# Optimization experiments

Hardware: AMD Instinct MI355X
Metric: run time of the kernel (lower is better)

Reference implementation:

```python
import jax, jax.numpy as jnp
import numpy as np

EPS = 1e-5
TOP_K = 2


def setup_inputs() -> dict:
    key = jax.random.key(0)
    ks = jax.random.split(key, 6)
    T, H, F, E = 4096, 1024, 2816, 8
    scale = 0.02
    return {
        "hidden_states": jax.random.normal(ks[0], (T, H), dtype=jnp.float32),
        "ln_w": jnp.ones((H,), dtype=jnp.float32),
        "router_w": jax.random.normal(ks[1], (H, E), dtype=jnp.float32) * scale,
        "w_gate": jax.random.normal(ks[2], (E, H, F), dtype=jnp.float32) * scale,
        "w_up": jax.random.normal(ks[3], (E, H, F), dtype=jnp.float32) * scale,
        "w_down": jax.random.normal(ks[4], (E, F, H), dtype=jnp.float32) * scale,
    }


def reference(hidden_states, ln_w, router_w, w_gate, w_up, w_down):
    # RMSNorm (LlamaRMSNorm)
    var = jnp.mean(hidden_states * hidden_states, axis=-1, keepdims=True)
    x = hidden_states * jax.lax.rsqrt(var + EPS) * ln_w  # [T, H]

    # TopKRouter: softmax over experts, then top-k probs/indices
    logits = x @ router_w                     # [T, E]
    probs = jax.nn.softmax(logits, axis=-1)
    topk_p, topk_i = jax.lax.top_k(probs, TOP_K)  # [T, K]

    # Dense combine weights [T, E]: prob for routed experts, 0 otherwise
    T = x.shape[0]
    combine = jnp.zeros_like(probs).at[jnp.arange(T)[:, None], topk_i].add(topk_p)

    # Experts: Llama-style gated MLP (SwiGLU); loop over fixed small expert set
    out = jnp.zeros_like(x)
    for e in range(w_gate.shape[0]):
        h = jax.nn.silu(x @ w_gate[e]) * (x @ w_up[e])   # [T, F]
        out = out + combine[:, e:e + 1] * (h @ w_down[e])
    return out
```

## Files before the change

### kernel.cpp

```cpp
#include <hip/hip_runtime.h>

#define T_TOK 4096
#define H_DIM 1024
#define F_DIM 2816
#define E_NUM 8
#define EPSV 1e-5f

typedef unsigned short u16;
typedef __attribute__((ext_vector_type(8))) short bf16x8;
typedef __attribute__((ext_vector_type(4))) float f32x4;

__device__ __forceinline__ u16 f2bf(float f) {
  union { float f; unsigned u; } c; c.f = f;
  unsigned u = c.u;
  return (u16)((u + 0x7FFFu + ((u >> 16) & 1u)) >> 16);
}

__global__ __launch_bounds__(256) void router_kernel(
    const float* __restrict__ hs, const float* __restrict__ lnw,
    const float* __restrict__ rw, u16* __restrict__ x_h,
    int* __restrict__ cnt, int* __restrict__ list,
    float* __restrict__ wcomb, int* __restrict__ slot) {
  const int wave = threadIdx.x >> 6;
  const int lane = threadIdx.x & 63;
  const int t = blockIdx.x * 4 + wave;
  const float* row = hs + (size_t)t * H_DIM;

  float4 v[4];
  float ss = 0.f;
#pragma unroll
  for (int j = 0; j < 4; ++j) {
    v[j] = ((const float4*)row)[j * 64 + lane];
    ss += v[j].x * v[j].x + v[j].y * v[j].y + v[j].z * v[j].z + v[j].w * v[j].w;
  }
#pragma unroll
  for (int m = 32; m; m >>= 1) ss += __shfl_xor(ss, m, 64);
  const float inv = rsqrtf(ss * (1.0f / H_DIM) + EPSV);

  float lg[E_NUM];
#pragma unroll
  for (int e = 0; e < E_NUM; ++e) lg[e] = 0.f;

#pragma unroll
  for (int j = 0; j < 4; ++j) {
    const int idx = j * 64 + lane;
    const int h0 = idx * 4;
    float4 w4 = ((const float4*)lnw)[idx];
    float xv[4] = {v[j].x * inv * w4.x, v[j].y * inv * w4.y,
                   v[j].z * inv * w4.z, v[j].w * inv * w4.w};
    ushort4 xs;
    xs.x = f2bf(xv[0]); xs.y = f2bf(xv[1]); xs.z = f2bf(xv[2]); xs.w = f2bf(xv[3]);
    ((ushort4*)(x_h + (size_t)t * H_DIM))[idx] = xs;
#pragma unroll
    for (int q = 0; q < 4; ++q) {
      const float* rr = rw + (size_t)(h0 + q) * E_NUM;
      float4 a = ((const float4*)rr)[0];
      float4 b = ((const float4*)rr)[1];
      lg[0] += xv[q] * a.x; lg[1] += xv[q] * a.y;
      lg[2] += xv[q] * a.z; lg[3] += xv[q] * a.w;
      lg[4] += xv[q] * b.x; lg[5] += xv[q] * b.y;
      lg[6] += xv[q] * b.z; lg[7] += xv[q] * b.w;
    }
  }
#pragma unroll
  for (int e = 0; e < E_NUM; ++e)
#pragma unroll
    for (int m = 32; m; m >>= 1) lg[e] += __shfl_xor(lg[e], m, 64);

  if (lane == 0) {
    float mx = lg[0];
#pragma unroll
    for (int e = 1; e < E_NUM; ++e) mx = fmaxf(mx, lg[e]);
    float p[E_NUM], s = 0.f;
#pragma unroll
    for (int e = 0; e < E_NUM; ++e) { p[e] = __expf(lg[e] - mx); s += p[e]; }
    const float invs = 1.0f / s;
    int e1 = 0; float b1 = p[0];
#pragma unroll
    for (int e = 1; e < E_NUM; ++e) if (p[e] > b1) { b1 = p[e]; e1 = e; }
    int e2 = -1; float b2 = -1.f;
#pragma unroll
    for (int e = 0; e < E_NUM; ++e) if (e != e1 && p[e] > b2) { b2 = p[e]; e2 = e; }
    b1 *= invs; b2 *= invs;
    int p1 = atomicAdd(&cnt[e1], 1);
    list[e1 * T_TOK + p1] = t; wcomb[e1 * T_TOK + p1] = b1;
    slot[2 * t] = (e1 << 16) | p1;
    int p2 = atomicAdd(&cnt[e2], 1);
    list[e2 * T_TOK + p2] = t; wcomb[e2 * T_TOK + p2] = b2;
    slot[2 * t + 1] = (e2 << 16) | p2;
  }
}

__global__ void offsets_kernel(const int* __restrict__ cnt, int* __restrict__ offs) {
  if (threadIdx.x == 0) {
    int s = 0;
    for (int e = 0; e < E_NUM; ++e) { offs[e] = s; s += cnt[e]; }
  }
}

__global__ __launch_bounds__(256) void transpose_cvt(
    const float* __restrict__ in, u16* __restrict__ out, int R, int C) {
  __shared__ float tile[32][33];
  const size_t base = (size_t)blockIdx.z * R * C;
  const int c0 = blockIdx.x * 32, r0 = blockIdx.y * 32;
  const int tx = threadIdx.x, ty = threadIdx.y;
#pragma unroll
  for (int j = 0; j < 32; j += 8)
    tile[ty + j][tx] = in[base + (size_t)(r0 + ty + j) * C + c0 + tx];
  __syncthreads();
#pragma unroll
  for (int j = 0; j < 32; j += 8)
    out[base + (size_t)(c0 + ty + j) * R + r0 + tx] = f2bf(tile[tx][ty + j]);
}

__global__ __launch_bounds__(256) void gemm1_kernel(
    const u16* __restrict__ x_h, const u16* __restrict__ wgT,
    const u16* __restrict__ wuT, const int* __restrict__ cnt,
    const int* __restrict__ offs, const int* __restrict__ list,
    u16* __restrict__ hbuf) {
  const int e = blockIdx.z;
  const int n_e = cnt[e];
  const int rt = blockIdx.y;
  if (rt * 128 >= n_e) return;
  const int ft = blockIdx.x;

  __shared__ __align__(16) u16 As[128][72];
  __shared__ __align__(16) u16 Bgs[64][72];
  __shared__ __align__(16) u16 Bus[64][72];
  __shared__ int tok[128];

  const int tid = threadIdx.x;
  if (tid < 128) {
    int r = rt * 128 + tid;
    if (r >= n_e) r = n_e - 1;
    tok[tid] = list[e * T_TOK + r];
  }
  __syncthreads();

  const int wv = tid >> 6, lane = tid & 63;
  const int wm = wv >> 1, wn = wv & 1;
  const int lrow = lane & 15, quad = lane >> 4;

  f32x4 accg[4][2], accu[4][2];
#pragma unroll
  for (int i = 0; i < 4; ++i)
#pragma unroll
    for (int j = 0; j < 2; ++j) {
      accg[i][j] = f32x4{0.f, 0.f, 0.f, 0.f};
      accu[i][j] = f32x4{0.f, 0.f, 0.f, 0.f};
    }

  const size_t wb = ((size_t)e * F_DIM + (size_t)ft * 64) * H_DIM;

  for (int k0 = 0; k0 < H_DIM; k0 += 64) {
#pragma unroll
    for (int i = 0; i < 4; ++i) {
      int c = tid + i * 256;
      int r = c >> 3, kc = (c & 7) << 3;
      *(uint4*)&As[r][kc] = *(const uint4*)(x_h + (size_t)tok[r] * H_DIM + k0 + kc);
    }
#pragma unroll
    for (int i = 0; i < 2; ++i) {
      int c = tid + i * 256;
      int fr = c >> 3, kc = (c & 7) << 3;
      size_t g = wb + (size_t)fr * H_DIM + k0 + kc;
      *(uint4*)&Bgs[fr][kc] = *(const uint4*)(wgT + g);
      *(uint4*)&Bus[fr][kc] = *(const uint4*)(wuT + g);
    }
    __syncthreads();
#pragma unroll
    for (int ks = 0; ks < 2; ++ks) {
      const int kk = ks * 32 + quad * 8;
      bf16x8 a[4], bg[2], bu[2];
#pragma unroll
      for (int tm = 0; tm < 4; ++tm)
        a[tm] = *(const bf16x8*)&As[wm * 64 + tm * 16 + lrow][kk];
#pragma unroll
      for (int tn = 0; tn < 2; ++tn) {
        bg[tn] = *(const bf16x8*)&Bgs[wn * 32 + tn * 16 + lrow][kk];
        bu[tn] = *(const bf16x8*)&Bus[wn * 32 + tn * 16 + lrow][kk];
      }
#pragma unroll
      for (int tm = 0; tm < 4; ++tm)
#pragma unroll
        for (int tn = 0; tn < 2; ++tn) {
          accg[tm][tn] = __builtin_amdgcn_mfma_f32_16x16x32_bf16(a[tm], bg[tn], accg[tm][tn], 0, 0, 0);
          accu[tm][tn] = __builtin_amdgcn_mfma_f32_16x16x32_bf16(a[tm], bu[tn], accu[tm][tn], 0, 0, 0);
        }
    }
    __syncthreads();
  }

  const int oe = offs[e];
#pragma unroll
  for (int tm = 0; tm < 4; ++tm) {
    const int lr0 = wm * 64 + tm * 16 + quad * 4;
#pragma unroll
    for (int rr = 0; rr < 4; ++rr) {
      const int gr = rt * 128 + lr0 + rr;
      if (gr < n_e) {
#pragma unroll
        for (int tn = 0; tn < 2; ++tn) {
          float g = accg[tm][tn][rr];
          float u = accu[tm][tn][rr];
          float hv = g / (1.0f + __expf(-g)) * u;
          int col = ft * 64 + wn * 32 + tn * 16 + lrow;
          hbuf[(size_t)(oe + gr) * F_DIM + col] = f2bf(hv);
        }
      }
    }
  }
}

__global__ __launch_bounds__(256) void gemm2_kernel(
    const u16* __restrict__ hbuf, const u16* __restrict__ wdT,
    const int* __restrict__ cnt, const int* __restrict__ offs,
    const float* __restrict__ wcomb, float* __restrict__ contrib) {
  const int e = blockIdx.z;
  const int n_e = cnt[e];
  const int rt = blockIdx.y;
  if (rt * 128 >= n_e) return;
  const int nt = blockIdx.x;

  __shared__ __align__(16) u16 As[128][72];
  __shared__ __align__(16) u16 Bs[64][72];
  __shared__ int hrow[128];

  const int tid = threadIdx.x;
  const int oe = offs[e];
  if (tid < 128) {
    int r = rt * 128 + tid;
    if (r >= n_e) r = n_e - 1;
    hrow[tid] = oe + r;
  }
  __syncthreads();

  const int wv = tid >> 6, lane = tid & 63;
  const int wm = wv >> 1, wn = wv & 1;
  const int lrow = lane & 15, quad = lane >> 4;

  f32x4 acc[4][2];
#pragma unroll
  for (int i = 0; i < 4; ++i)
#pragma unroll
    for (int j = 0; j < 2; ++j) acc[i][j] = f32x4{0.f, 0.f, 0.f, 0.f};

  const size_t wb = ((size_t)e * H_DIM + (size_t)nt * 64) * F_DIM;

  for (int k0 = 0; k0 < F_DIM; k0 += 64) {
#pragma unroll
    for (int i = 0; i < 4; ++i) {
      int c = tid + i * 256;
      int r = c >> 3, kc = (c & 7) << 3;
      *(uint4*)&As[r][kc] = *(const uint4*)(hbuf + (size_t)hrow[r] * F_DIM + k0 + kc);
    }
#pragma unroll
    for (int i = 0; i < 2; ++i) {
      int c = tid + i * 256;
      int fr = c >> 3, kc = (c & 7) << 3;
      *(uint4*)&Bs[fr][kc] = *(const uint4*)(wdT + wb + (size_t)fr * F_DIM + k0 + kc);
    }
    __syncthreads();
#pragma unroll
    for (int ks = 0; ks < 2; ++ks) {
      const int kk = ks * 32 + quad * 8;
      bf16x8 a[4], b[2];
#pragma unroll
      for (int tm = 0; tm < 4; ++tm)
        a[tm] = *(const bf16x8*)&As[wm * 64 + tm * 16 + lrow][kk];
#pragma unroll
      for (int tn = 0; tn < 2; ++tn)
        b[tn] = *(const bf16x8*)&Bs[wn * 32 + tn * 16 + lrow][kk];
#pragma unroll
      for (int tm = 0; tm < 4; ++tm)
#pragma unroll
        for (int tn = 0; tn < 2; ++tn)
          acc[tm][tn] = __builtin_amdgcn_mfma_f32_16x16x32_bf16(a[tm], b[tn], acc[tm][tn], 0, 0, 0);
    }
    __syncthreads();
  }

#pragma unroll
  for (int tm = 0; tm < 4; ++tm) {
    const int lr0 = wm * 64 + tm * 16 + quad * 4;
#pragma unroll
    for (int rr = 0; rr < 4; ++rr) {
      const int gr = rt * 128 + lr0 + rr;
      if (gr < n_e) {
        const float cw = wcomb[e * T_TOK + gr];
#pragma unroll
        for (int tn = 0; tn < 2; ++tn) {
          int col = nt * 64 + wn * 32 + tn * 16 + lrow;
          contrib[(size_t)(oe + gr) * H_DIM + col] = acc[tm][tn][rr] * cw;
        }
      }
    }
  }
}

__global__ __launch_bounds__(256) void combine_kernel(
    const float* __restrict__ contrib, const int* __restrict__ offs,
    const int* __restrict__ slot, float* __restrict__ out) {
  const int t = blockIdx.x;
  const int s0 = slot[2 * t], s1 = slot[2 * t + 1];
  const int r0 = offs[s0 >> 16] + (s0 & 0xFFFF);
  const int r1 = offs[s1 >> 16] + (s1 & 0xFFFF);
  float4 a = ((const float4*)(contrib + (size_t)r0 * H_DIM))[threadIdx.x];
  float4 b = ((const float4*)(contrib + (size_t)r1 * H_DIM))[threadIdx.x];
  float4 o = {a.x + b.x, a.y + b.y, a.z + b.z, a.w + b.w};
  ((float4*)(out + (size_t)t * H_DIM))[threadIdx.x] = o;
}

extern "C" void kernel_launch(void* const* d_in, const int* in_sizes, int n_in,
                              void* d_out, int out_size, void* d_ws, size_t ws_size,
                              hipStream_t stream) {
  const float* hs  = (const float*)d_in[0];
  const float* lnw = (const float*)d_in[1];
  const float* rw  = (const float*)d_in[2];
  const float* wg  = (const float*)d_in[3];
  const float* wu  = (const float*)d_in[4];
  const float* wd  = (const float*)d_in[5];
  float* out = (float*)d_out;

  char* p = (char*)d_ws;
  const size_t SZ_XH = (size_t)T_TOK * H_DIM * 2;
  const size_t SZ_W  = (size_t)E_NUM * F_DIM * H_DIM * 2;
  const size_t SZ_HB = (size_t)T_TOK * 2 * F_DIM * 2;
  const size_t SZ_CT = (size_t)T_TOK * 2 * H_DIM * 4;

  u16* x_h  = (u16*)p;   p += SZ_XH;
  u16* wgT  = (u16*)p;   p += SZ_W;
  u16* wuT  = (u16*)p;   p += SZ_W;
  u16* wdT  = (u16*)p;   p += SZ_W;
  u16* hbuf = (u16*)p;   p += SZ_HB;
  float* contrib = (float*)p; p += SZ_CT;
  int* cnt  = (int*)p;   p += 256;
  int* offs = (int*)p;   p += 256;
  int* list = (int*)p;   p += (size_t)E_NUM * T_TOK * 4;
  float* wcomb = (float*)p; p += (size_t)E_NUM * T_TOK * 4;
  int* slot = (int*)p;   p += (size_t)T_TOK * 2 * 4;

  hipMemsetAsync(cnt, 0, 256, stream);
  router_kernel<<<T_TOK / 4, 256, 0, stream>>>(hs, lnw, rw, x_h, cnt, list, wcomb, slot);
  offsets_kernel<<<1, 64, 0, stream>>>(cnt, offs);
  transpose_cvt<<<dim3(F_DIM / 32, H_DIM / 32, E_NUM), dim3(32, 8), 0, stream>>>(wg, wgT, H_DIM, F_DIM);
  transpose_cvt<<<dim3(F_DIM / 32, H_DIM / 32, E_NUM), dim3(32, 8), 0, stream>>>(wu, wuT, H_DIM, F_DIM);
  transpose_cvt<<<dim3(H_DIM / 32, F_DIM / 32, E_NUM), dim3(32, 8), 0, stream>>>(wd, wdT, F_DIM, H_DIM);
  gemm1_kernel<<<dim3(F_DIM / 64, T_TOK / 128, E_NUM), 256, 0, stream>>>(x_h, wgT, wuT, cnt, offs, list, hbuf);
  gemm2_kernel<<<dim3(H_DIM / 64, T_TOK / 128, E_NUM), 256, 0, stream>>>(hbuf, wdT, cnt, offs, wcomb, contrib);
  combine_kernel<<<T_TOK, 256, 0, stream>>>(contrib, offs, slot, out);
}
```

Baseline: 673.6 us.

## Rework MoE GEMMs with 32x32 MFMA, LDS direct loads, swizzle, atomic combine

Both expert GEMMs now use 128x128 tiles with 32x32x16 bf16 MFMA, fill shared memory through global_load_lds direct loads, and address it with an XOR-swizzled layout in place of padded rows. The three weight transposes become one fused launch using 64x64 tiles with vectorized reads and writes. The combine kernel and the contrib buffer are removed: gemm2 atomically adds weighted results straight into a zeroed output. The aim is higher MFMA throughput, less staging overhead and fewer launches and passes over memory, at the cost of nondeterministic float atomics and a larger register footprint.

```diff
diff --git a/kernel.cpp b/kernel.cpp
--- a/kernel.cpp
+++ b/kernel.cpp
@@ -8,7 +8,8 @@
 
 typedef unsigned short u16;
 typedef __attribute__((ext_vector_type(8))) short bf16x8;
-typedef __attribute__((ext_vector_type(4))) float f32x4;
+typedef __attribute__((ext_vector_type(16))) float f32x16;
+typedef __attribute__((ext_vector_type(8))) u16 u16x8;
 
 __device__ __forceinline__ u16 f2bf(float f) {
   union { float f; unsigned u; } c; c.f = f;
@@ -16,11 +17,17 @@
   return (u16)((u + 0x7FFFu + ((u >> 16) & 1u)) >> 16);
 }
 
+__device__ __forceinline__ void llds16(const u16* g, u16* l) {
+  __builtin_amdgcn_global_load_lds(
+      (const __attribute__((address_space(1))) unsigned int*)g,
+      (__attribute__((address_space(3))) unsigned int*)l, 16, 0, 0);
+}
+
 __global__ __launch_bounds__(256) void router_kernel(
     const float* __restrict__ hs, const float* __restrict__ lnw,
     const float* __restrict__ rw, u16* __restrict__ x_h,
     int* __restrict__ cnt, int* __restrict__ list,
-    float* __restrict__ wcomb, int* __restrict__ slot) {
+    float* __restrict__ wcomb) {
   const int wave = threadIdx.x >> 6;
   const int lane = threadIdx.x & 63;
   const int t = blockIdx.x * 4 + wave;
@@ -84,10 +91,8 @@
     b1 *= invs; b2 *= invs;
     int p1 = atomicAdd(&cnt[e1], 1);
     list[e1 * T_TOK + p1] = t; wcomb[e1 * T_TOK + p1] = b1;
-    slot[2 * t] = (e1 << 16) | p1;
     int p2 = atomicAdd(&cnt[e2], 1);
     list[e2 * T_TOK + p2] = t; wcomb[e2 * T_TOK + p2] = b2;
-    slot[2 * t + 1] = (e2 << 16) | p2;
   }
 }
 
@@ -98,19 +103,48 @@
   }
 }
 
-__global__ __launch_bounds__(256) void transpose_cvt(
-    const float* __restrict__ in, u16* __restrict__ out, int R, int C) {
-  __shared__ float tile[32][33];
-  const size_t base = (size_t)blockIdx.z * R * C;
-  const int c0 = blockIdx.x * 32, r0 = blockIdx.y * 32;
-  const int tx = threadIdx.x, ty = threadIdx.y;
-#pragma unroll
-  for (int j = 0; j < 32; j += 8)
-    tile[ty + j][tx] = in[base + (size_t)(r0 + ty + j) * C + c0 + tx];
+__global__ __launch_bounds__(256) void transpose_fused(
+    const float* __restrict__ wg, const float* __restrict__ wu,
+    const float* __restrict__ wd, u16* __restrict__ wgT,
+    u16* __restrict__ wuT, u16* __restrict__ wdT) {
+  __shared__ float tile[64 * 65];
+  const int bid = blockIdx.x;
+  const int seg = bid / 5632;
+  const int rem = bid - seg * 5632;
+  const int e = rem / 704;
+  const int tt = rem - e * 704;
+  int R, C, rt, ct;
+  const float* in; u16* outp;
+  if (seg < 2) {
+    R = H_DIM; C = F_DIM; rt = tt / 44; ct = tt - rt * 44;
+    in = seg ? wu : wg; outp = seg ? wuT : wgT;
+  } else {
+    R = F_DIM; C = H_DIM; rt = tt / 16; ct = tt - rt * 16;
+    in = wd; outp = wdT;
+  }
+  const size_t base = (size_t)e * R * C;
+  const int r0 = rt * 64, c0 = ct * 64;
+  const int tid = threadIdx.x;
+  const int rr = tid >> 4, cv = tid & 15;
+#pragma unroll
+  for (int p = 0; p < 4; ++p) {
+    int r = p * 16 + rr;
+    float4 v = *(const float4*)(in + base + (size_t)(r0 + r) * C + c0 + cv * 4);
+    tile[r * 65 + cv * 4 + 0] = v.x;
+    tile[r * 65 + cv * 4 + 1] = v.y;
+    tile[r * 65 + cv * 4 + 2] = v.z;
+    tile[r * 65 + cv * 4 + 3] = v.w;
+  }
   __syncthreads();
 #pragma unroll
-  for (int j = 0; j < 32; j += 8)
-    out[base + (size_t)(c0 + ty + j) * R + r0 + tx] = f2bf(tile[tx][ty + j]);
+  for (int q = 0; q < 2; ++q) {
+    int id = q * 256 + tid;
+    int c = id >> 3, rc = id & 7;
+    u16x8 o;
+#pragma unroll
+    for (int j = 0; j < 8; ++j) o[j] = f2bf(tile[(rc * 8 + j) * 65 + c]);
+    *(u16x8*)(outp + base + (size_t)(c0 + c) * R + r0 + rc * 8) = o;
+  }
 }
 
 __global__ __launch_bounds__(256) void gemm1_kernel(
@@ -124,9 +158,9 @@
   if (rt * 128 >= n_e) return;
   const int ft = blockIdx.x;
 
-  __shared__ __align__(16) u16 As[128][72];
-  __shared__ __align__(16) u16 Bgs[64][72];
-  __shared__ __align__(16) u16 Bus[64][72];
+  __shared__ __align__(16) u16 As[128 * 64];
+  __shared__ __align__(16) u16 Bgs[128 * 64];
+  __shared__ __align__(16) u16 Bus[128 * 64];
   __shared__ int tok[128];
 
   const int tid = threadIdx.x;
@@ -139,53 +173,60 @@
 
   const int wv = tid >> 6, lane = tid & 63;
   const int wm = wv >> 1, wn = wv & 1;
-  const int lrow = lane & 15, quad = lane >> 4;
-
-  f32x4 accg[4][2], accu[4][2];
-#pragma unroll
-  for (int i = 0; i < 4; ++i)
+  const int l31 = lane & 31, kh = lane >> 5, l7 = lane & 7;
+  const int sr = lane >> 3;
+  const int sw = (l7 ^ sr) << 3;
+
+  const size_t wb = ((size_t)e * F_DIM + (size_t)ft * 128) * H_DIM;
+  const u16* agp[4]; const u16* bgp[4]; const u16* bup[4];
+#pragma unroll
+  for (int i = 0; i < 4; ++i) {
+    int r = wv * 32 + i * 8 + sr;
+    agp[i] = x_h + (size_t)tok[r] * H_DIM + sw;
+    bgp[i] = wgT + wb + (size_t)r * H_DIM + sw;
+    bup[i] = wuT + wb + (size_t)r * H_DIM + sw;
+  }
+
+  int arow[2], brow[2];
+#pragma unroll
+  for (int t = 0; t < 2; ++t) {
+    arow[t] = (wm * 64 + t * 32 + l31) * 64;
+    brow[t] = (wn * 64 + t * 32 + l31) * 64;
+  }
+
+  f32x16 accg[2][2], accu[2][2];
+#pragma unroll
+  for (int i = 0; i < 2; ++i)
 #pragma unroll
     for (int j = 0; j < 2; ++j) {
-      accg[i][j] = f32x4{0.f, 0.f, 0.f, 0.f};
-      accu[i][j] = f32x4{0.f, 0.f, 0.f, 0.f};
-    }
-
-  const size_t wb = ((size_t)e * F_DIM + (size_t)ft * 64) * H_DIM;
+      accg[i][j] = (f32x16)(0.f);
+      accu[i][j] = (f32x16)(0.f);
+    }
 
   for (int k0 = 0; k0 < H_DIM; k0 += 64) {
 #pragma unroll
     for (int i = 0; i < 4; ++i) {
-      int c = tid + i * 256;
-      int r = c >> 3, kc = (c & 7) << 3;
-      *(uint4*)&As[r][kc] = *(const uint4*)(x_h + (size_t)tok[r] * H_DIM + k0 + kc);
-    }
-#pragma unroll
-    for (int i = 0; i < 2; ++i) {
-      int c = tid + i * 256;
-      int fr = c >> 3, kc = (c & 7) << 3;
-      size_t g = wb + (size_t)fr * H_DIM + k0 + kc;
-      *(uint4*)&Bgs[fr][kc] = *(const uint4*)(wgT + g);
-      *(uint4*)&Bus[fr][kc] = *(const uint4*)(wuT + g);
+      llds16(agp[i] + k0, &As[(wv * 32 + i * 8) * 64]);
+      llds16(bgp[i] + k0, &Bgs[(wv * 32 + i * 8) * 64]);
+      llds16(bup[i] + k0, &Bus[(wv * 32 + i * 8) * 64]);
     }
     __syncthreads();
 #pragma unroll
-    for (int ks = 0; ks < 2; ++ks) {
-      const int kk = ks * 32 + quad * 8;
-      bf16x8 a[4], bg[2], bu[2];
-#pragma unroll
-      for (int tm = 0; tm < 4; ++tm)
-        a[tm] = *(const bf16x8*)&As[wm * 64 + tm * 16 + lrow][kk];
-#pragma unroll
-      for (int tn = 0; tn < 2; ++tn) {
-        bg[tn] = *(const bf16x8*)&Bgs[wn * 32 + tn * 16 + lrow][kk];
-        bu[tn] = *(const bf16x8*)&Bus[wn * 32 + tn * 16 + lrow][kk];
+    for (int ks = 0; ks < 4; ++ks) {
+      const int cho = (((ks * 2) | kh) ^ l7) << 3;
+      bf16x8 a[2], bg[2], bu[2];
+#pragma unroll
+      for (int t = 0; t < 2; ++t) {
+        a[t]  = *(const bf16x8*)&As [arow[t] + cho];
+        bg[t] = *(const bf16x8*)&Bgs[brow[t] + cho];
+        bu[t] = *(const bf16x8*)&Bus[brow[t] + cho];
       }
 #pragma unroll
-      for (int tm = 0; tm < 4; ++tm)
+      for (int tm = 0; tm < 2; ++tm)
 #pragma unroll
         for (int tn = 0; tn < 2; ++tn) {
-          accg[tm][tn] = __builtin_amdgcn_mfma_f32_16x16x32_bf16(a[tm], bg[tn], accg[tm][tn], 0, 0, 0);
-          accu[tm][tn] = __builtin_amdgcn_mfma_f32_16x16x32_bf16(a[tm], bu[tn], accu[tm][tn], 0, 0, 0);
+          accg[tm][tn] = __builtin_amdgcn_mfma_f32_32x32x16_bf16(a[tm], bg[tn], accg[tm][tn], 0, 0, 0);
+          accu[tm][tn] = __builtin_amdgcn_mfma_f32_32x32x16_bf16(a[tm], bu[tn], accu[tm][tn], 0, 0, 0);
         }
     }
     __syncthreads();
@@ -193,37 +234,37 @@
 
   const int oe = offs[e];
 #pragma unroll
-  for (int tm = 0; tm < 4; ++tm) {
-    const int lr0 = wm * 64 + tm * 16 + quad * 4;
-#pragma unroll
-    for (int rr = 0; rr < 4; ++rr) {
-      const int gr = rt * 128 + lr0 + rr;
+  for (int tm = 0; tm < 2; ++tm)
+#pragma unroll
+    for (int rg = 0; rg < 16; ++rg) {
+      const int rowi = (rg & 3) + 8 * (rg >> 2) + 4 * kh;
+      const int gr = rt * 128 + wm * 64 + tm * 32 + rowi;
       if (gr < n_e) {
+        const size_t ob = (size_t)(oe + gr) * F_DIM + ft * 128 + wn * 64 + l31;
 #pragma unroll
         for (int tn = 0; tn < 2; ++tn) {
-          float g = accg[tm][tn][rr];
-          float u = accu[tm][tn][rr];
+          float g = accg[tm][tn][rg];
+          float u = accu[tm][tn][rg];
           float hv = g / (1.0f + __expf(-g)) * u;
-          int col = ft * 64 + wn * 32 + tn * 16 + lrow;
-          hbuf[(size_t)(oe + gr) * F_DIM + col] = f2bf(hv);
+          hbuf[ob + tn * 32] = f2bf(hv);
         }
       }
     }
-  }
 }
 
 __global__ __launch_bounds__(256) void gemm2_kernel(
     const u16* __restrict__ hbuf, const u16* __restrict__ wdT,
     const int* __restrict__ cnt, const int* __restrict__ offs,
-    const float* __restrict__ wcomb, float* __restrict__ contrib) {
+    const int* __restrict__ list, const float* __restrict__ wcomb,
+    float* __restrict__ out) {
   const int e = blockIdx.z;
   const int n_e = cnt[e];
   const int rt = blockIdx.y;
   if (rt * 128 >= n_e) return;
   const int nt = blockIdx.x;
 
-  __shared__ __align__(16) u16 As[128][72];
-  __shared__ __align__(16) u16 Bs[64][72];
+  __shared__ __align__(16) u16 As[128 * 64];
+  __shared__ __align__(16) u16 Bs[128 * 64];
   __shared__ int hrow[128];
 
   const int tid = threadIdx.x;
@@ -237,78 +278,72 @@
 
   const int wv = tid >> 6, lane = tid & 63;
   const int wm = wv >> 1, wn = wv & 1;
-  const int lrow = lane & 15, quad = lane >> 4;
-
-  f32x4 acc[4][2];
-#pragma unroll
-  for (int i = 0; i < 4; ++i)
-#pragma unroll
-    for (int j = 0; j < 2; ++j) acc[i][j] = f32x4{0.f, 0.f, 0.f, 0.f};
-
-  const size_t wb = ((size_t)e * H_DIM + (size_t)nt * 64) * F_DIM;
+  const int l31 = lane & 31, kh = lane >> 5, l7 = lane & 7;
+  const int sr = lane >> 3;
+  const int sw = (l7 ^ sr) << 3;
+
+  const size_t wb = ((size_t)e * H_DIM + (size_t)nt * 128) * F_DIM;
+  const u16* agp[4]; const u16* bgp[4];
+#pragma unroll
+  for (int i = 0; i < 4; ++i) {
+    int r = wv * 32 + i * 8 + sr;
+    agp[i] = hbuf + (size_t)hrow[r] * F_DIM + sw;
+    bgp[i] = wdT + wb + (size_t)r * F_DIM + sw;
+  }
+
+  int arow[2], brow[2];
+#pragma unroll
+  for (int t = 0; t < 2; ++t) {
+    arow[t] = (wm * 64 + t * 32 + l31) * 64;
+    brow[t] = (wn * 64 + t * 32 + l31) * 64;
+  }
+
+  f32x16 acc[2][2];
+#pragma unroll
+  for (int i = 0; i < 2; ++i)
+#pragma unroll
+    for (int j = 0; j < 2; ++j) acc[i][j] = (f32x16)(0.f);
 
   for (int k0 = 0; k0 < F_DIM; k0 += 64) {
 #pragma unroll
     for (int i = 0; i < 4; ++i) {
-      int c = tid + i * 256;
-      int r = c >> 3, kc = (c & 7) << 3;
-      *(uint4*)&As[r][kc] = *(const uint4*)(hbuf + (size_t)hrow[r] * F_DIM + k0 + kc);
-    }
-#pragma unroll
-    for (int i = 0; i < 2; ++i) {
-      int c = tid + i * 256;
-      int fr = c >> 3, kc = (c & 7) << 3;
-      *(uint4*)&Bs[fr][kc] = *(const uint4*)(wdT + wb + (size_t)fr * F_DIM + k0 + kc);
+      llds16(agp[i] + k0, &As[(wv * 32 + i * 8) * 64]);
+      llds16(bgp[i] + k0, &Bs[(wv * 32 + i * 8) * 64]);
     }
     __syncthreads();
 #pragma unroll
-    for (int ks = 0; ks < 2; ++ks) {
-      const int kk = ks * 32 + quad * 8;
-      bf16x8 a[4], b[2];
-#pragma unroll
-      for (int tm = 0; tm < 4; ++tm)
-        a[tm] = *(const bf16x8*)&As[wm * 64 + tm * 16 + lrow][kk];
-#pragma unroll
-      for (int tn = 0; tn < 2; ++tn)
-        b[tn] = *(const bf16x8*)&Bs[wn * 32 + tn * 16 + lrow][kk];
-#pragma unroll
-      for (int tm = 0; tm < 4; ++tm)
+    for (int ks = 0; ks < 4; ++ks) {
+      const int cho = (((ks * 2) | kh) ^ l7) << 3;
+      bf16x8 a[2], b[2];
+#pragma unroll
+      for (int t = 0; t < 2; ++t) {
+        a[t] = *(const bf16x8*)&As[arow[t] + cho];
+        b[t] = *(const bf16x8*)&Bs[brow[t] + cho];
+      }
+#pragma unroll
+      for (int tm = 0; tm < 2; ++tm)
 #pragma unroll
         for (int tn = 0; tn < 2; ++tn)
-          acc[tm][tn] = __builtin_amdgcn_mfma_f32_16x16x32_bf16(a[tm], b[tn], acc[tm][tn], 0, 0, 0);
+          acc[tm][tn] = __builtin_amdgcn_mfma_f32_32x32x16_bf16(a[tm], b[tn], acc[tm][tn], 0, 0, 0);
     }
     __syncthreads();
   }
 
 #pragma unroll
-  for (int tm = 0; tm < 4; ++tm) {
-    const int lr0 = wm * 64 + tm * 16 + quad * 4;
-#pragma unroll
-    for (int rr = 0; rr < 4; ++rr) {
-      const int gr = rt * 128 + lr0 + rr;
+  for (int tm = 0; tm < 2; ++tm)
+#pragma unroll
+    for (int rg = 0; rg < 16; ++rg) {
+      const int rowi = (rg & 3) + 8 * (rg >> 2) + 4 * kh;
+      const int gr = rt * 128 + wm * 64 + tm * 32 + rowi;
       if (gr < n_e) {
+        const int t = list[e * T_TOK + gr];
         const float cw = wcomb[e * T_TOK + gr];
-#pragma unroll
-        for (int tn = 0; tn < 2; ++tn) {
-          int col = nt * 64 + wn * 32 + tn * 16 + lrow;
-          contrib[(size_t)(oe + gr) * H_DIM + col] = acc[tm][tn][rr] * cw;
-        }
+        float* ob = out + (size_t)t * H_DIM + nt * 128 + wn * 64 + l31;
+#pragma unroll
+        for (int tn = 0; tn < 2; ++tn)
+          atomicAdd(ob + tn * 32, acc[tm][tn][rg] * cw);
       }
     }
-  }
-}
-
-__global__ __launch_bounds__(256) void combine_kernel(
-    const float* __restrict__ contrib, const int* __restrict__ offs,
-    const int* __restrict__ slot, float* __restrict__ out) {
-  const int t = blockIdx.x;
-  const int s0 = slot[2 * t], s1 = slot[2 * t + 1];
-  const int r0 = offs[s0 >> 16] + (s0 & 0xFFFF);
-  const int r1 = offs[s1 >> 16] + (s1 & 0xFFFF);
-  float4 a = ((const float4*)(contrib + (size_t)r0 * H_DIM))[threadIdx.x];
-  float4 b = ((const float4*)(contrib + (size_t)r1 * H_DIM))[threadIdx.x];
-  float4 o = {a.x + b.x, a.y + b.y, a.z + b.z, a.w + b.w};
-  ((float4*)(out + (size_t)t * H_DIM))[threadIdx.x] = o;
 }
 
 extern "C" void kernel_launch(void* const* d_in, const int* in_sizes, int n_in,
@@ -326,27 +361,22 @@
   const size_t SZ_XH = (size_t)T_TOK * H_DIM * 2;
   const size_t SZ_W  = (size_t)E_NUM * F_DIM * H_DIM * 2;
   const size_t SZ_HB = (size_t)T_TOK * 2 * F_DIM * 2;
-  const size_t SZ_CT = (size_t)T_TOK * 2 * H_DIM * 4;
 
   u16* x_h  = (u16*)p;   p += SZ_XH;
   u16* wgT  = (u16*)p;   p += SZ_W;
   u16* wuT  = (u16*)p;   p += SZ_W;
   u16* wdT  = (u16*)p;   p += SZ_W;
   u16* hbuf = (u16*)p;   p += SZ_HB;
-  float* contrib = (float*)p; p += SZ_CT;
   int* cnt  = (int*)p;   p += 256;
   int* offs = (int*)p;   p += 256;
   int* list = (int*)p;   p += (size_t)E_NUM * T_TOK * 4;
   float* wcomb = (float*)p; p += (size_t)E_NUM * T_TOK * 4;
-  int* slot = (int*)p;   p += (size_t)T_TOK * 2 * 4;
 
   hipMemsetAsync(cnt, 0, 256, stream);
-  router_kernel<<<T_TOK / 4, 256, 0, stream>>>(hs, lnw, rw, x_h, cnt, list, wcomb, slot);
+  hipMemsetAsync(out, 0, (size_t)out_size * 4, stream);
+  router_kernel<<<T_TOK / 4, 256, 0, stream>>>(hs, lnw, rw, x_h, cnt, list, wcomb);
   offsets_kernel<<<1, 64, 0, stream>>>(cnt, offs);
-  transpose_cvt<<<dim3(F_DIM / 32, H_DIM / 32, E_NUM), dim3(32, 8), 0, stream>>>(wg, wgT, H_DIM, F_DIM);
-  transpose_cvt<<<dim3(F_DIM / 32, H_DIM / 32, E_NUM), dim3(32, 8), 0, stream>>>(wu, wuT, H_DIM, F_DIM);
-  transpose_cvt<<<dim3(H_DIM / 32, F_DIM / 32, E_NUM), dim3(32, 8), 0, stream>>>(wd, wdT, F_DIM, H_DIM);
-  gemm1_kernel<<<dim3(F_DIM / 64, T_TOK / 128, E_NUM), 256, 0, stream>>>(x_h, wgT, wuT, cnt, offs, list, hbuf);
-  gemm2_kernel<<<dim3(H_DIM / 64, T_TOK / 128, E_NUM), 256, 0, stream>>>(hbuf, wdT, cnt, offs, wcomb, contrib);
-  combine_kernel<<<T_TOK, 256, 0, stream>>>(contrib, offs, slot, out);
-}
+  transpose_fused<<<3 * 5632, 256, 0, stream>>>(wg, wu, wd, wgT, wuT, wdT);
+  gemm1_kernel<<<dim3(F_DIM / 128, T_TOK / 128, E_NUM), 256, 0, stream>>>(x_h, wgT, wuT, cnt, offs, list, hbuf);
+  gemm2_kernel<<<dim3(H_DIM / 128, T_TOK / 128, E_NUM), 256, 0, stream>>>(hbuf, wdT, cnt, offs, list, wcomb, out);
+}
```

After: 725.3 us. +7.7%, slower.
